# Optimization experiments

Hardware: AMD Instinct MI355X
Metric: run time of the kernel (lower is better)

Reference implementation:

```python
import jax, jax.numpy as jnp
import numpy as np

N_ELEC, N_NUC, D, F, E = 1024, 256, 64, 64, 131072
HH, HG = 128, 128
# labels: en (elec->nuc), ne (nuc->elec), same (elec->elec), anti (elec->elec)
SRC_N = [N_ELEC, N_NUC, N_ELEC, N_ELEC]
TGT_N = [N_NUC, N_ELEC, N_ELEC, N_ELEC]


def setup_inputs() -> dict:
    key = jax.random.key(0)
    ks = jax.random.split(key, 16)
    s_elec = jax.random.normal(ks[0], (N_ELEC, D), jnp.float32)
    v_elec = jax.random.normal(ks[1], (N_ELEC, D, 3), jnp.float32)
    s_nuc = jax.random.normal(ks[2], (N_NUC, D), jnp.float32)
    v_nuc = jax.random.normal(ks[3], (N_NUC, D, 3), jnp.float32)
    senders = jnp.stack([jax.random.randint(jax.random.fold_in(ks[4], i), (E,), 0, SRC_N[i]) for i in range(4)]).astype(jnp.int32)
    receivers = jnp.stack([jax.random.randint(jax.random.fold_in(ks[5], i), (E,), 0, TGT_N[i]) for i in range(4)]).astype(jnp.int32)
    dist = jax.random.uniform(ks[6], (4, E, F), jnp.float32)
    dirs = jax.random.normal(ks[7], (4, E, 3), jnp.float32)
    dirs = dirs / jnp.linalg.norm(dirs, axis=-1, keepdims=True)  # unit directions
    def w_init(k, shape):
        return jax.random.normal(k, shape, jnp.float32) / jnp.sqrt(jnp.float32(shape[-2]))
    return {
        's_elec': s_elec, 'v_elec': v_elec, 's_nuc': s_nuc, 'v_nuc': v_nuc,
        'dist': dist, 'dirs': dirs,
        'W_w': w_init(ks[8], (4, F, 3 * D)),
        'W_h1': w_init(ks[9], (4, D, HH)), 'W_h2': w_init(ks[10], (4, HH, 3 * D)),
        'W_g1': w_init(ks[11], (4, 2 * D, HG)), 'W_g2': w_init(ks[12], (4, HG, 3 * D)),
        'W_V': jnp.broadcast_to(jnp.eye(D, dtype=jnp.float32), (4, D, D)),
        'W_U': jnp.broadcast_to(jnp.eye(D, dtype=jnp.float32), (4, D, D)),
        'senders': senders, 'receivers': receivers,
    }


def _painn_layer(s_elec, v_elec, s_nuc, v_nuc, dist, dirs, W_w, W_h1, W_h2, W_g1, W_g2, W_V, W_U, senders, receivers):
    src_s = [s_elec, s_nuc, s_elec, s_elec]
    src_v = [v_elec, v_nuc, v_elec, v_elec]
    ds_e = jnp.zeros_like(s_elec); dv_e = jnp.zeros_like(v_elec)
    ds_n = jnp.zeros_like(s_nuc); dv_n = jnp.zeros_like(v_nuc)
    for i in range(4):
        n_tgt = TGT_N[i]
        # edge MLPs: w (1-layer, last linear) and h (2-layer silu, last linear), bias-free
        we = dist[i] @ W_w[i]                                   # [E, 3D]
        h_all = jax.nn.silu(src_s[i] @ W_h1[i]) @ W_h2[i]        # [n_src, 3D]
        hx = h_all[senders[i]]                                   # gather per edge
        phi_s, phi_vv, phi_vs = jnp.split(we * hx, 3, axis=-1)   # each [E, D]
        z_s = jax.ops.segment_sum(phi_s, receivers[i], n_tgt)    # [n_tgt, D]
        vv = phi_vv[..., None] * src_v[i][senders[i]]            # [E, D, 3]
        vs = phi_vs[..., None] * dirs[i][:, None, :]             # [E, D, 3]
        z_v = jax.ops.segment_sum(vv + vs, receivers[i], n_tgt)  # [n_tgt, D, 3]
        Vv = jnp.einsum('ndi,df->nfi', z_v, W_V[i])
        Uv = jnp.einsum('ndi,df->nfi', z_v, W_U[i])
        g_in = jnp.concatenate([z_s, (Vv ** 2).sum(axis=-1)], axis=-1)  # [n_tgt, 2D]
        gs = jax.nn.silu(g_in @ W_g1[i]) @ W_g2[i]               # [n_tgt, 3D]
        a_ss, a_vv, a_sv = jnp.split(gs, 3, axis=-1)
        upd_v = Uv * a_vv[..., None]
        upd_s = a_sv * jnp.einsum('nfi,nfi->nf', Uv, Vv) + a_ss
        if i == 0:  # 'en' -> nuclei
            ds_n = ds_n + upd_s; dv_n = dv_n + upd_v
        else:       # 'ne','same','anti' -> electrons
            ds_e = ds_e + upd_s; dv_e = dv_e + upd_v
    s_e = s_elec + ds_e
    v_e = v_elec + dv_e
    return jnp.concatenate([s_e, v_e.reshape(N_ELEC, -1)], axis=-1)


def reference(s_elec, v_elec, s_nuc, v_nuc, dist, dirs, W_w, W_h1, W_h2, W_g1, W_g2, W_V, W_U, senders, receivers):
    return _painn_layer(s_elec, v_elec, s_nuc, v_nuc, dist, dirs, W_w, W_h1, W_h2, W_g1, W_g2, W_V, W_U, senders, receivers)
```

## Files before the change

kernel.cpp:

```cpp
#include <hip/hip_runtime.h>
#include <stdint.h>

#define E_EDGES 131072
#define NELEC 1024
#define NNUC 256
#define MAXCHUNK 256
#define NBLK 16

typedef unsigned short ushort_t;
typedef __attribute__((ext_vector_type(8))) short short8;
typedef __attribute__((ext_vector_type(4))) short short4_t;
typedef __attribute__((ext_vector_type(4))) float float4_t;
typedef __attribute__((ext_vector_type(4))) int int4_t;
typedef __attribute__((ext_vector_type(2))) unsigned int uint2_t;

__device__ inline float silu_f(float x){ return x / (1.0f + expf(-x)); }

__device__ inline short f2bf_rne(float x){
    union { float f; uint32_t u; } a; a.f = x;
    return (short)((a.u + 0x7fffu + ((a.u >> 16) & 1u)) >> 16);
}
__device__ inline float bf2f(short h){
    union { uint32_t u; float f; } a; a.u = ((uint32_t)(uint16_t)h) << 16;
    return a.f;
}
__device__ inline ushort_t bfu(float x){ return (ushort_t)f2bf_rne(x); }
__device__ inline float asf_lo(uint32_t u){ union { uint32_t u; float f; } a; a.u = u << 16; return a.f; }
__device__ inline float asf_hi(uint32_t u){ union { uint32_t u; float f; } a; a.u = u & 0xFFFF0000u; return a.f; }

__global__ __launch_bounds__(256) void prep_kernel(
    const float* __restrict__ s_elec, const float* __restrict__ v_elec,
    const float* __restrict__ s_nuc,  const float* __restrict__ v_nuc,
    const float* __restrict__ W_h1, const float* __restrict__ W_h2,
    const float* __restrict__ W_w,
    const int* __restrict__ receivers,
    ushort_t* __restrict__ tabA, ushort_t* __restrict__ tabB,
    short* __restrict__ fragH, short* __restrict__ fragL,
    int* __restrict__ bh, float* __restrict__ out)
{
    int b = blockIdx.x, tid = threadIdx.x;
    __shared__ float sls[8][64];
    __shared__ float hidls[128][8];
    __shared__ int hist[1024];

    if (b < 288){
        int t, node0;
        if (b < 32){ t = 0; node0 = b*8; }
        else if (b < 160){ t = 1; node0 = (b-32)*8; }
        else { t = 2; node0 = (b-160)*8; }
        int tp = t + 1;
        const float* src = (t == 0) ? s_nuc : s_elec;
        const float* vsrc = (t == 0) ? v_nuc : v_elec;
        long baseA = (t == 0) ? 0 : (t == 1 ? 32768 : 163840);
        long baseB = (t == 0) ? 0 : (t == 1 ? 65536 : 327680);
        for (int i = tid; i < 512; i += 256){ int n = i >> 6, f = i & 63; sls[n][f] = src[(node0+n)*64 + f]; }
        __syncthreads();
        {
            int j = tid & 127, nh = tid >> 7;
            const float* w1 = W_h1 + (long)tp*64*128;
            float a0=0,a1=0,a2=0,a3=0;
            #pragma unroll 8
            for (int f = 0; f < 64; f++){
                float w = w1[f*128 + j];
                a0 += sls[nh*4+0][f]*w; a1 += sls[nh*4+1][f]*w;
                a2 += sls[nh*4+2][f]*w; a3 += sls[nh*4+3][f]*w;
            }
            float4_t hv = { silu_f(a0), silu_f(a1), silu_f(a2), silu_f(a3) };
            *(float4_t*)&hidls[j][nh*4] = hv;
        }
        __syncthreads();
        if (tid < 192){
            const float* w2 = W_h2 + (long)tp*128*192;
            float acc[8] = {0,0,0,0,0,0,0,0};
            #pragma unroll 4
            for (int h = 0; h < 128; h++){
                float w = w2[h*192 + tid];
                float4_t ha = *(float4_t*)&hidls[h][0];
                float4_t hb = *(float4_t*)&hidls[h][4];
                acc[0]+=ha[0]*w; acc[1]+=ha[1]*w; acc[2]+=ha[2]*w; acc[3]+=ha[3]*w;
                acc[4]+=hb[0]*w; acc[5]+=hb[1]*w; acc[6]+=hb[2]*w; acc[7]+=hb[3]*w;
            }
            int p = tid >> 6, d2 = tid & 63;
            if (p == 0){
                #pragma unroll
                for (int n = 0; n < 8; n++)
                    tabA[baseA + (long)((node0+n)*64 + d2)*2 + 0] = bfu(acc[n]);
            } else if (p == 2){
                #pragma unroll
                for (int n = 0; n < 8; n++)
                    tabA[baseA + (long)((node0+n)*64 + d2)*2 + 1] = bfu(acc[n]);
            } else {
                #pragma unroll
                for (int n = 0; n < 8; n++){
                    const float* vp = vsrc + (long)(node0+n)*192 + d2*3;
                    long o = baseB + (long)((node0+n)*64 + d2)*4;
                    tabB[o+0] = bfu(acc[n]*vp[0]);
                    tabB[o+1] = bfu(acc[n]*vp[1]);
                    tabB[o+2] = bfu(acc[n]*vp[2]);
                }
            }
        }
    } else if (b < 291){
        int t = b - 288, tp = t + 1;
        const float* W = W_w + (long)tp*64*192;
        for (int idx = tid; idx < 12288; idx += 256){
            int j    = idx & 7;
            int lane = (idx >> 3) & 63;
            int ks   = (idx >> 9) & 1;
            int nt   = idx >> 10;
            int k = ks*32 + ((lane >> 4) & 3)*8 + j;
            int n = nt*16 + (lane & 15);
            float v = W[k*192 + n];
            short hi = f2bf_rne(v);
            short lo = f2bf_rne(v - bf2f(hi));
            fragH[t*12288 + idx] = hi;
            fragL[t*12288 + idx] = lo;
        }
    } else if (b < 547){
        int i = (b - 291)*256 + tid;
        int n = i >> 6, c4 = i & 63;
        float4_t v;
        if (c4 < 16) v = *(const float4_t*)(s_elec + n*64 + c4*4);
        else         v = *(const float4_t*)(v_elec + n*192 + (c4-16)*4);
        *(float4_t*)(out + n*256 + c4*4) = v;
    } else {
        int hb = b - 547, t = hb >> 4, blk = hb & 15;
        for (int i = tid; i < 1024; i += 256) hist[i] = 0;
        __syncthreads();
        long base = (long)(t+1)*E_EDGES + blk*8192;
        #pragma unroll 4
        for (int it = 0; it < 32; it++){
            int r = receivers[base + it*256 + tid];
            atomicAdd(&hist[r], 1);
        }
        __syncthreads();
        for (int bin = tid; bin < 1024; bin += 256)
            bh[(t*1024 + bin)*NBLK + blk] = hist[bin];
    }
}

__global__ __launch_bounds__(1024) void scan_kernel(int* __restrict__ bh,
                                                    int* __restrict__ offs,
                                                    int* __restrict__ counts){
    __shared__ int buf[1024];
    int tid = threadIdx.x;
    int base = tid*48;
    int vals[48];
    const int4_t* p = (const int4_t*)(bh + base);
    int s = 0;
    #pragma unroll
    for (int j = 0; j < 12; j++){
        int4_t x = p[j];
        vals[j*4+0]=x[0]; vals[j*4+1]=x[1]; vals[j*4+2]=x[2]; vals[j*4+3]=x[3];
        s += x[0]+x[1]+x[2]+x[3];
    }
    buf[tid] = s;
    __syncthreads();
    int x = s;
    for (int off = 1; off < 1024; off <<= 1){
        int y = (tid >= off) ? buf[tid - off] : 0;
        __syncthreads();
        x += y; buf[tid] = x;
        __syncthreads();
    }
    int run = x - s;
    #pragma unroll
    for (int k = 0; k < 3; k++){
        int tb = tid*3 + k;
        offs[tb] = run;
        int c = 0;
        #pragma unroll
        for (int j = 0; j < 16; j++){
            int v = vals[k*16 + j];
            bh[base + k*16 + j] = run;
            run += v; c += v;
        }
        counts[tb] = c;
    }
}

__global__ __launch_bounds__(256) void scatter_kernel(const int* __restrict__ receivers,
                                                      const int* __restrict__ senders,
                                                      const int* __restrict__ bh,
                                                      int* __restrict__ sorted){
    int hb = blockIdx.x, t = hb >> 4, blk = hb & 15;
    int tid = threadIdx.x;
    __shared__ int cur[1024];
    for (int bin = tid; bin < 1024; bin += 256) cur[bin] = bh[(t*1024 + bin)*NBLK + blk];
    __syncthreads();
    long base = (long)(t+1)*E_EDGES + blk*8192;
    #pragma unroll 2
    for (int it = 0; it < 32; it++){
        int e = blk*8192 + it*256 + tid;
        int r = receivers[base + it*256 + tid];
        int snd = senders[base + it*256 + tid];
        int pos = atomicAdd(&cur[r], 1);
        sorted[pos] = e | (snd << 17);
    }
}

__global__ __launch_bounds__(256) void main_kernel(
    const float* __restrict__ dist, const float* __restrict__ dirs,
    const float* __restrict__ W_V, const float* __restrict__ W_U,
    const float* __restrict__ W_g1, const float* __restrict__ W_g2,
    const ushort_t* __restrict__ tabA, const ushort_t* __restrict__ tabB,
    const short* __restrict__ fragH, const short* __restrict__ fragL,
    const int* __restrict__ counts, const int* __restrict__ offs, const int* __restrict__ sorted,
    float* __restrict__ out)
{
    int b = blockIdx.x;
    int t = b >> 10, node = b & 1023, tp = t + 1;
    const ushort_t* ta = tabA + ((t == 0) ? 0 : (t == 1 ? 32768 : 163840));
    const ushort_t* tb = tabB + ((t == 0) ? 0 : (t == 1 ? 65536 : 327680));
    const float* dbase = dist + (long)tp*E_EDGES*64;
    const float* dirbase = dirs + (long)tp*E_EDGES*3;

    int tid = threadIdx.x;
    int w = tid >> 6, l = tid & 63;
    int q = l >> 4, c16 = l & 15;
    int d = w*16 + c16;

    __shared__ short AH[2][2][64][8];
    __shared__ short AL[2][2][64][8];
    __shared__ float dls[2][16][3];
    __shared__ int eid[MAXCHUNK];
    __shared__ int sid[MAXCHUNK];
    __shared__ float zs[64];
    __shared__ float zv[64][3];
    __shared__ float VvL[192], UvL[192];
    __shared__ float gin[128], hidl[128], aL[192], vdotL[64];

    short8 bhf[3][2], blf[3][2];
    #pragma unroll
    for (int ni = 0; ni < 3; ni++){
        int nt = w + ni*4;
        #pragma unroll
        for (int ks = 0; ks < 2; ks++){
            long base = (long)t*12288 + ((nt*2 + ks)*64 + l)*8;
            bhf[ni][ks] = *(const short8*)(fragH + base);
            blf[ni][ks] = *(const short8*)(fragL + base);
        }
    }

    float acc_s = 0.f, acc_v0 = 0.f, acc_v1 = 0.f, acc_v2 = 0.f;

    int deg   = counts[t*1024 + node];
    int start = offs[t*1024 + node];

    int m = tid >> 4, seg = tid & 15;
    int ks_w = seg >> 3, quad_w = (seg >> 1) & 3, j0_w = (seg & 1)*4;
    int lane2 = m | (quad_w << 4);
    int mm = tid / 3, ii = tid - mm*3;

    const float4_t z4 = {0.f,0.f,0.f,0.f};

    for (int cbase = 0; cbase < deg; cbase += MAXCHUNK){
        int chunk = deg - cbase; if (chunk > MAXCHUNK) chunk = MAXCHUNK;
        __syncthreads();
        {
            int v = 0;
            if (tid < chunk) v = sorted[(long)start + cbase + tid];
            eid[tid] = v & 131071;
            sid[tid] = ((unsigned)v) >> 17;
        }
        __syncthreads();

        int ngroups = (chunk + 15) >> 4;
        float4_t dv = z4;
        if (m < chunk) dv = *(const float4_t*)(dbase + (long)eid[m]*64 + seg*4);
        float dirv = 0.f;
        if (tid < 48 && mm < chunk) dirv = dirbase[(long)eid[mm]*3 + ii];
        uint32_t gA[4]; uint2_t gB[4];
        #pragma unroll
        for (int r = 0; r < 4; r++){
            int s = sid[q*4 + r];
            gA[r] = *(const uint32_t*)(ta + (long)(s*64 + d)*2);
            gB[r] = *(const uint2_t*)(tb + (long)(s*64 + d)*4);
        }

        for (int g = 0; g < ngroups; g++){
            int buf = g & 1;
            {
                short4_t h4, l4;
                #pragma unroll
                for (int jj = 0; jj < 4; jj++){
                    short hi = f2bf_rne(dv[jj]);
                    h4[jj] = hi;
                    l4[jj] = f2bf_rne(dv[jj] - bf2f(hi));
                }
                *(short4_t*)&AH[buf][ks_w][lane2][j0_w] = h4;
                *(short4_t*)&AL[buf][ks_w][lane2][j0_w] = l4;
                if (tid < 48) dls[buf][mm][ii] = dirv;
            }
            float4_t dvn = z4; float dirn = 0.f;
            uint32_t gAn[4] = {0,0,0,0}; uint2_t gBn[4] = {{0,0},{0,0},{0,0},{0,0}};
            if (g + 1 < ngroups){
                int li = (g+1)*16 + m;
                if (li < chunk) dvn = *(const float4_t*)(dbase + (long)eid[li]*64 + seg*4);
                int li2 = (g+1)*16 + mm;
                if (tid < 48 && li2 < chunk) dirn = dirbase[(long)eid[li2]*3 + ii];
                #pragma unroll
                for (int r = 0; r < 4; r++){
                    int s = sid[(g+1)*16 + q*4 + r];
                    gAn[r] = *(const uint32_t*)(ta + (long)(s*64 + d)*2);
                    gBn[r] = *(const uint2_t*)(tb + (long)(s*64 + d)*4);
                }
            }
            __syncthreads();

            short8 ah0 = *(short8*)&AH[buf][0][l][0];
            short8 ah1 = *(short8*)&AH[buf][1][l][0];
            short8 al0 = *(short8*)&AL[buf][0][l][0];
            short8 al1 = *(short8*)&AL[buf][1][l][0];
            float4_t C[3];
            #pragma unroll
            for (int ni = 0; ni < 3; ni++){
                float4_t acc = z4;
                acc = __builtin_amdgcn_mfma_f32_16x16x32_bf16(ah0, bhf[ni][0], acc, 0, 0, 0);
                acc = __builtin_amdgcn_mfma_f32_16x16x32_bf16(ah1, bhf[ni][1], acc, 0, 0, 0);
                acc = __builtin_amdgcn_mfma_f32_16x16x32_bf16(ah0, blf[ni][0], acc, 0, 0, 0);
                acc = __builtin_amdgcn_mfma_f32_16x16x32_bf16(ah1, blf[ni][1], acc, 0, 0, 0);
                acc = __builtin_amdgcn_mfma_f32_16x16x32_bf16(al0, bhf[ni][0], acc, 0, 0, 0);
                acc = __builtin_amdgcn_mfma_f32_16x16x32_bf16(al1, bhf[ni][1], acc, 0, 0, 0);
                C[ni] = acc;
            }

            #pragma unroll
            for (int r = 0; r < 4; r++){
                int mr = q*4 + r;
                float hs  = asf_lo(gA[r]);
                float hvs = asf_hi(gA[r]);
                float hv0 = asf_lo(gB[r][0]);
                float hv1 = asf_hi(gB[r][0]);
                float hv2 = asf_lo(gB[r][1]);
                acc_s += C[0][r] * hs;
                float pvs = C[2][r] * hvs;
                acc_v0 += C[1][r]*hv0 + pvs * dls[buf][mr][0];
                acc_v1 += C[1][r]*hv1 + pvs * dls[buf][mr][1];
                acc_v2 += C[1][r]*hv2 + pvs * dls[buf][mr][2];
            }
            dv = dvn; dirv = dirn;
            #pragma unroll
            for (int r = 0; r < 4; r++){ gA[r] = gAn[r]; gB[r] = gBn[r]; }
        }
    }

    acc_s  += __shfl_xor(acc_s, 16);  acc_s  += __shfl_xor(acc_s, 32);
    acc_v0 += __shfl_xor(acc_v0, 16); acc_v0 += __shfl_xor(acc_v0, 32);
    acc_v1 += __shfl_xor(acc_v1, 16); acc_v1 += __shfl_xor(acc_v1, 32);
    acc_v2 += __shfl_xor(acc_v2, 16); acc_v2 += __shfl_xor(acc_v2, 32);
    __syncthreads();
    if (l < 16){
        zs[d] = acc_s;
        zv[d][0] = acc_v0; zv[d][1] = acc_v1; zv[d][2] = acc_v2;
    }
    __syncthreads();

    if (tid < 192){
        int i = tid >> 6, f = tid & 63;
        const float* wv = W_V + (long)tp*64*64;
        const float* wu = W_U + (long)tp*64*64;
        float av = 0.f, au = 0.f;
        #pragma unroll 8
        for (int dd = 0; dd < 64; dd++){
            float z = zv[dd][i];
            av += z * wv[dd*64 + f];
            au += z * wu[dd*64 + f];
        }
        VvL[f*3 + i] = av;
        UvL[f*3 + i] = au;
    }
    __syncthreads();
    if (tid < 64){
        int f = tid;
        float v0 = VvL[f*3], v1 = VvL[f*3+1], v2 = VvL[f*3+2];
        float u0 = UvL[f*3], u1 = UvL[f*3+1], u2 = UvL[f*3+2];
        gin[f] = zs[f];
        gin[64 + f] = v0*v0 + v1*v1 + v2*v2;
        vdotL[f] = u0*v0 + u1*v1 + u2*v2;
    }
    __syncthreads();
    if (tid < 128){
        const float* w1 = W_g1 + (long)tp*128*128;
        float acc = 0.f;
        #pragma unroll 8
        for (int c = 0; c < 128; c++) acc += gin[c] * w1[c*128 + tid];
        hidl[tid] = silu_f(acc);
    }
    __syncthreads();
    if (tid < 192){
        const float* w2 = W_g2 + (long)tp*128*192;
        float acc = 0.f;
        #pragma unroll 8
        for (int h = 0; h < 128; h++) acc += hidl[h] * w2[h*192 + tid];
        aL[tid] = acc;
    }
    __syncthreads();
    if (tid < 64){
        int f = tid;
        float upd = aL[128 + f] * vdotL[f] + aL[f];
        atomicAdd(&out[node*256 + f], upd);
    }
    if (tid < 192){
        int i = tid >> 6, f = tid & 63;
        float updv = UvL[f*3 + i] * aL[64 + f];
        atomicAdd(&out[node*256 + 64 + f*3 + i], updv);
    }
}

extern "C" void kernel_launch(void* const* d_in, const int* in_sizes, int n_in,
                              void* d_out, int out_size, void* d_ws, size_t ws_size,
                              hipStream_t stream){
    const float* s_elec  = (const float*)d_in[0];
    const float* v_elec  = (const float*)d_in[1];
    const float* s_nuc   = (const float*)d_in[2];
    const float* v_nuc   = (const float*)d_in[3];
    const float* dist    = (const float*)d_in[4];
    const float* dirs    = (const float*)d_in[5];
    const float* W_w     = (const float*)d_in[6];
    const float* W_h1    = (const float*)d_in[7];
    const float* W_h2    = (const float*)d_in[8];
    const float* W_g1    = (const float*)d_in[9];
    const float* W_g2    = (const float*)d_in[10];
    const float* W_V     = (const float*)d_in[11];
    const float* W_U     = (const float*)d_in[12];
    const int* senders   = (const int*)d_in[13];
    const int* receivers = (const int*)d_in[14];
    float* out = (float*)d_out;
    char* ws = (char*)d_ws;

    ushort_t* tabA  = (ushort_t*)(ws + 0);
    ushort_t* tabB  = (ushort_t*)(ws + 589824);
    short* fragH  = (short*)(ws + 1769472);
    short* fragL  = (short*)(ws + 1843200);
    int*   bh     = (int*)  (ws + 1916928);
    int*   offs   = (int*)  (ws + 2113536);
    int*   counts = (int*)  (ws + 2125824);
    int*   sorted = (int*)  (ws + 2138112);
    if (ws_size < 3710976) return;

    prep_kernel<<<dim3(595), dim3(256), 0, stream>>>(
        s_elec, v_elec, s_nuc, v_nuc, W_h1, W_h2, W_w, receivers,
        tabA, tabB, fragH, fragL, bh, out);
    scan_kernel<<<dim3(1), dim3(1024), 0, stream>>>(bh, offs, counts);
    scatter_kernel<<<dim3(48), dim3(256), 0, stream>>>(receivers, senders, bh, sorted);
    main_kernel<<<dim3(3072), dim3(256), 0, stream>>>(
        dist, dirs, W_V, W_U, W_g1, W_g2,
        tabA, tabB, fragH, fragL, counts, offs, sorted, out);
}
```

Baseline: 365.3 us.

## Split main kernel into edge aggregation and batched node update kernels

Splits the per-node main kernel into two: an edge kernel that gathers and aggregates messages into a z buffer in workspace, and an update kernel that runs the V/U projections and gate MLP for four nodes per block, so each weight load is reused across nodes. The scan is also spread over three blocks, one per edge type, in place of a single block. The aim is to take the serial per-node MLP tail off the edge-heavy blocks and to amortise weight reads. In exchange it adds a kernel launch and a round trip through global memory, and the split path runs only when the workspace is large enough.

```diff
diff --git a/kernel.cpp b/kernel.cpp
--- a/kernel.cpp
+++ b/kernel.cpp
@@ -6,6 +6,7 @@
 #define NNUC 256
 #define MAXCHUNK 256
 #define NBLK 16
+#define UNPB 4
 
 typedef unsigned short ushort_t;
 typedef __attribute__((ext_vector_type(8))) short short8;
@@ -143,13 +144,14 @@
                                                     int* __restrict__ offs,
                                                     int* __restrict__ counts){
     __shared__ int buf[1024];
+    int t = blockIdx.x;
     int tid = threadIdx.x;
-    int base = tid*48;
-    int vals[48];
+    int base = (t*1024 + tid)*NBLK;
+    int vals[NBLK];
     const int4_t* p = (const int4_t*)(bh + base);
     int s = 0;
     #pragma unroll
-    for (int j = 0; j < 12; j++){
+    for (int j = 0; j < NBLK/4; j++){
         int4_t x = p[j];
         vals[j*4+0]=x[0]; vals[j*4+1]=x[1]; vals[j*4+2]=x[2]; vals[j*4+3]=x[3];
         s += x[0]+x[1]+x[2]+x[3];
@@ -163,19 +165,13 @@
         x += y; buf[tid] = x;
         __syncthreads();
     }
-    int run = x - s;
+    int run = t*E_EDGES + (x - s);
+    offs[t*1024 + tid] = run;
+    counts[t*1024 + tid] = s;
     #pragma unroll
-    for (int k = 0; k < 3; k++){
-        int tb = tid*3 + k;
-        offs[tb] = run;
-        int c = 0;
-        #pragma unroll
-        for (int j = 0; j < 16; j++){
-            int v = vals[k*16 + j];
-            bh[base + k*16 + j] = run;
-            run += v; c += v;
-        }
-        counts[tb] = c;
+    for (int j = 0; j < NBLK; j++){
+        bh[base + j] = run;
+        run += vals[j];
     }
 }
 
@@ -196,6 +192,253 @@
         int snd = senders[base + it*256 + tid];
         int pos = atomicAdd(&cur[r], 1);
         sorted[pos] = e | (snd << 17);
+    }
+}
+
+__global__ __launch_bounds__(256) void edge_kernel(
+    const float* __restrict__ dist, const float* __restrict__ dirs,
+    const ushort_t* __restrict__ tabA, const ushort_t* __restrict__ tabB,
+    const short* __restrict__ fragH, const short* __restrict__ fragL,
+    const int* __restrict__ counts, const int* __restrict__ offs, const int* __restrict__ sorted,
+    float* __restrict__ zbuf)
+{
+    int b = blockIdx.x;
+    int t = b >> 10, node = b & 1023, tp = t + 1;
+    const ushort_t* ta = tabA + ((t == 0) ? 0 : (t == 1 ? 32768 : 163840));
+    const ushort_t* tb = tabB + ((t == 0) ? 0 : (t == 1 ? 65536 : 327680));
+    const float* dbase = dist + (long)tp*E_EDGES*64;
+    const float* dirbase = dirs + (long)tp*E_EDGES*3;
+
+    int tid = threadIdx.x;
+    int w = tid >> 6, l = tid & 63;
+    int q = l >> 4, c16 = l & 15;
+    int d = w*16 + c16;
+
+    __shared__ short AH[2][2][64][8];
+    __shared__ short AL[2][2][64][8];
+    __shared__ float dls[2][16][3];
+    __shared__ int eid[MAXCHUNK];
+    __shared__ int sid[MAXCHUNK];
+
+    short8 bhf[3][2], blf[3][2];
+    #pragma unroll
+    for (int ni = 0; ni < 3; ni++){
+        int nt = w + ni*4;
+        #pragma unroll
+        for (int ks = 0; ks < 2; ks++){
+            long base = (long)t*12288 + ((nt*2 + ks)*64 + l)*8;
+            bhf[ni][ks] = *(const short8*)(fragH + base);
+            blf[ni][ks] = *(const short8*)(fragL + base);
+        }
+    }
+
+    float acc_s = 0.f, acc_v0 = 0.f, acc_v1 = 0.f, acc_v2 = 0.f;
+
+    int deg   = counts[t*1024 + node];
+    int start = offs[t*1024 + node];
+
+    int m = tid >> 4, seg = tid & 15;
+    int ks_w = seg >> 3, quad_w = (seg >> 1) & 3, j0_w = (seg & 1)*4;
+    int lane2 = m | (quad_w << 4);
+    int mm = tid / 3, ii = tid - mm*3;
+
+    const float4_t z4 = {0.f,0.f,0.f,0.f};
+
+    for (int cbase = 0; cbase < deg; cbase += MAXCHUNK){
+        int chunk = deg - cbase; if (chunk > MAXCHUNK) chunk = MAXCHUNK;
+        __syncthreads();
+        {
+            int v = 0;
+            if (tid < chunk) v = sorted[(long)start + cbase + tid];
+            eid[tid] = v & 131071;
+            sid[tid] = ((unsigned)v) >> 17;
+        }
+        __syncthreads();
+
+        int ngroups = (chunk + 15) >> 4;
+        float4_t dv = z4;
+        if (m < chunk) dv = *(const float4_t*)(dbase + (long)eid[m]*64 + seg*4);
+        float dirv = 0.f;
+        if (tid < 48 && mm < chunk) dirv = dirbase[(long)eid[mm]*3 + ii];
+        uint32_t gA[4]; uint2_t gB[4];
+        #pragma unroll
+        for (int r = 0; r < 4; r++){
+            int s = sid[q*4 + r];
+            gA[r] = *(const uint32_t*)(ta + (long)(s*64 + d)*2);
+            gB[r] = *(const uint2_t*)(tb + (long)(s*64 + d)*4);
+        }
+
+        for (int g = 0; g < ngroups; g++){
+            int buf = g & 1;
+            {
+                short4_t h4, l4;
+                #pragma unroll
+                for (int jj = 0; jj < 4; jj++){
+                    short hi = f2bf_rne(dv[jj]);
+                    h4[jj] = hi;
+                    l4[jj] = f2bf_rne(dv[jj] - bf2f(hi));
+                }
+                *(short4_t*)&AH[buf][ks_w][lane2][j0_w] = h4;
+                *(short4_t*)&AL[buf][ks_w][lane2][j0_w] = l4;
+                if (tid < 48) dls[buf][mm][ii] = dirv;
+            }
+            float4_t dvn = z4; float dirn = 0.f;
+            uint32_t gAn[4] = {0,0,0,0}; uint2_t gBn[4] = {{0,0},{0,0},{0,0},{0,0}};
+            if (g + 1 < ngroups){
+                int li = (g+1)*16 + m;
+                if (li < chunk) dvn = *(const float4_t*)(dbase + (long)eid[li]*64 + seg*4);
+                int li2 = (g+1)*16 + mm;
+                if (tid < 48 && li2 < chunk) dirn = dirbase[(long)eid[li2]*3 + ii];
+                #pragma unroll
+                for (int r = 0; r < 4; r++){
+                    int s = sid[(g+1)*16 + q*4 + r];
+                    gAn[r] = *(const uint32_t*)(ta + (long)(s*64 + d)*2);
+                    gBn[r] = *(const uint2_t*)(tb + (long)(s*64 + d)*4);
+                }
+            }
+            __syncthreads();
+
+            short8 ah0 = *(short8*)&AH[buf][0][l][0];
+            short8 ah1 = *(short8*)&AH[buf][1][l][0];
+            short8 al0 = *(short8*)&AL[buf][0][l][0];
+            short8 al1 = *(short8*)&AL[buf][1][l][0];
+            float4_t C[3];
+            #pragma unroll
+            for (int ni = 0; ni < 3; ni++){
+                float4_t acc = z4;
+                acc = __builtin_amdgcn_mfma_f32_16x16x32_bf16(ah0, bhf[ni][0], acc, 0, 0, 0);
+                acc = __builtin_amdgcn_mfma_f32_16x16x32_bf16(ah1, bhf[ni][1], acc, 0, 0, 0);
+                acc = __builtin_amdgcn_mfma_f32_16x16x32_bf16(ah0, blf[ni][0], acc, 0, 0, 0);
+                acc = __builtin_amdgcn_mfma_f32_16x16x32_bf16(ah1, blf[ni][1], acc, 0, 0, 0);
+                acc = __builtin_amdgcn_mfma_f32_16x16x32_bf16(al0, bhf[ni][0], acc, 0, 0, 0);
+                acc = __builtin_amdgcn_mfma_f32_16x16x32_bf16(al1, bhf[ni][1], acc, 0, 0, 0);
+                C[ni] = acc;
+            }
+
+            #pragma unroll
+            for (int r = 0; r < 4; r++){
+                int mr = q*4 + r;
+                float hs  = asf_lo(gA[r]);
+                float hvs = asf_hi(gA[r]);
+                float hv0 = asf_lo(gB[r][0]);
+                float hv1 = asf_hi(gB[r][0]);
+                float hv2 = asf_lo(gB[r][1]);
+                acc_s += C[0][r] * hs;
+                float pvs = C[2][r] * hvs;
+                acc_v0 += C[1][r]*hv0 + pvs * dls[buf][mr][0];
+                acc_v1 += C[1][r]*hv1 + pvs * dls[buf][mr][1];
+                acc_v2 += C[1][r]*hv2 + pvs * dls[buf][mr][2];
+            }
+            dv = dvn; dirv = dirn;
+            #pragma unroll
+            for (int r = 0; r < 4; r++){ gA[r] = gAn[r]; gB[r] = gBn[r]; }
+        }
+    }
+
+    acc_s  += __shfl_xor(acc_s, 16);  acc_s  += __shfl_xor(acc_s, 32);
+    acc_v0 += __shfl_xor(acc_v0, 16); acc_v0 += __shfl_xor(acc_v0, 32);
+    acc_v1 += __shfl_xor(acc_v1, 16); acc_v1 += __shfl_xor(acc_v1, 32);
+    acc_v2 += __shfl_xor(acc_v2, 16); acc_v2 += __shfl_xor(acc_v2, 32);
+    if (l < 16){
+        float* zp = zbuf + ((long)(t*1024 + node))*256;
+        zp[d] = acc_s;
+        zp[64 + d*3 + 0] = acc_v0;
+        zp[64 + d*3 + 1] = acc_v1;
+        zp[64 + d*3 + 2] = acc_v2;
+    }
+}
+
+__global__ __launch_bounds__(256) void update_kernel(
+    const float* __restrict__ W_V, const float* __restrict__ W_U,
+    const float* __restrict__ W_g1, const float* __restrict__ W_g2,
+    const float* __restrict__ zbuf, float* __restrict__ out)
+{
+    int b = blockIdx.x;
+    int t = b >> 8, tp = t + 1;
+    int nb = (b & 255) * UNPB;
+    int tid = threadIdx.x;
+
+    __shared__ float zls[UNPB][256];
+    __shared__ float Vv[UNPB][64][3], Uv[UNPB][64][3];
+    __shared__ float gin[UNPB][128];
+    __shared__ float hid[UNPB][128];
+    __shared__ float aL[UNPB][192];
+    __shared__ float vdot[UNPB][64];
+
+    {
+        int n = tid >> 6, c = tid & 63;
+        *(float4_t*)&zls[n][c*4] =
+            *(const float4_t*)(zbuf + ((long)(t*1024 + nb + n))*256 + c*4);
+    }
+    __syncthreads();
+
+    {
+        int f = tid & 63, n = tid >> 6;
+        const float* wv = W_V + (long)tp*4096;
+        const float* wu = W_U + (long)tp*4096;
+        float av0=0,av1=0,av2=0,au0=0,au1=0,au2=0;
+        #pragma unroll 4
+        for (int dd = 0; dd < 64; dd++){
+            float wvv = wv[dd*64 + f], wuu = wu[dd*64 + f];
+            float z0 = zls[n][64 + dd*3 + 0];
+            float z1 = zls[n][64 + dd*3 + 1];
+            float z2 = zls[n][64 + dd*3 + 2];
+            av0 += z0*wvv; av1 += z1*wvv; av2 += z2*wvv;
+            au0 += z0*wuu; au1 += z1*wuu; au2 += z2*wuu;
+        }
+        Vv[n][f][0]=av0; Vv[n][f][1]=av1; Vv[n][f][2]=av2;
+        Uv[n][f][0]=au0; Uv[n][f][1]=au1; Uv[n][f][2]=au2;
+    }
+    __syncthreads();
+
+    {
+        int n = tid >> 6, f = tid & 63;
+        float v0=Vv[n][f][0], v1=Vv[n][f][1], v2=Vv[n][f][2];
+        float u0=Uv[n][f][0], u1=Uv[n][f][1], u2=Uv[n][f][2];
+        gin[n][f]      = zls[n][f];
+        gin[n][64 + f] = v0*v0 + v1*v1 + v2*v2;
+        vdot[n][f]     = u0*v0 + u1*v1 + u2*v2;
+    }
+    __syncthreads();
+
+    {
+        int h = tid & 127, ng = tid >> 7;
+        const float* w1 = W_g1 + (long)tp*16384;
+        float a0=0, a1=0;
+        #pragma unroll 4
+        for (int c = 0; c < 128; c++){
+            float w = w1[c*128 + h];
+            a0 += gin[ng*2+0][c]*w;
+            a1 += gin[ng*2+1][c]*w;
+        }
+        hid[ng*2+0][h] = silu_f(a0);
+        hid[ng*2+1][h] = silu_f(a1);
+    }
+    __syncthreads();
+
+    if (tid < 192){
+        const float* w2 = W_g2 + (long)tp*24576;
+        float a0=0,a1=0,a2=0,a3=0;
+        #pragma unroll 4
+        for (int h = 0; h < 128; h++){
+            float w = w2[h*192 + tid];
+            a0 += hid[0][h]*w; a1 += hid[1][h]*w;
+            a2 += hid[2][h]*w; a3 += hid[3][h]*w;
+        }
+        aL[0][tid]=a0; aL[1][tid]=a1; aL[2][tid]=a2; aL[3][tid]=a3;
+    }
+    __syncthreads();
+
+    {
+        int n = tid >> 6, f = tid & 63;
+        float upd = aL[n][128 + f]*vdot[n][f] + aL[n][f];
+        atomicAdd(&out[(nb + n)*256 + f], upd);
+        float g = aL[n][64 + f];
+        #pragma unroll
+        for (int i = 0; i < 3; i++){
+            float updv = Uv[n][f][i] * g;
+            atomicAdd(&out[(nb + n)*256 + 64 + f*3 + i], updv);
+        }
     }
 }
 
@@ -228,7 +471,7 @@
     __shared__ float zs[64];
     __shared__ float zv[64][3];
     __shared__ float VvL[192], UvL[192];
-    __shared__ float gin[128], hidl[128], aL[192], vdotL[64];
+    __shared__ float gin[128], hidl[128], aLrr[192], vdotL[64];
 
     short8 bhf[3][2], blf[3][2];
     #pragma unroll
@@ -393,17 +636,17 @@
         float acc = 0.f;
         #pragma unroll 8
         for (int h = 0; h < 128; h++) acc += hidl[h] * w2[h*192 + tid];
-        aL[tid] = acc;
+        aLrr[tid] = acc;
     }
     __syncthreads();
     if (tid < 64){
         int f = tid;
-        float upd = aL[128 + f] * vdotL[f] + aL[f];
+        float upd = aLrr[128 + f] * vdotL[f] + aLrr[f];
         atomicAdd(&out[node*256 + f], upd);
     }
     if (tid < 192){
         int i = tid >> 6, f = tid & 63;
-        float updv = UvL[f*3 + i] * aL[64 + f];
+        float updv = UvL[f*3 + i] * aLrr[64 + f];
         atomicAdd(&out[node*256 + 64 + f*3 + i], updv);
     }
 }
@@ -437,14 +680,23 @@
     int*   offs   = (int*)  (ws + 2113536);
     int*   counts = (int*)  (ws + 2125824);
     int*   sorted = (int*)  (ws + 2138112);
+    float* zbuf   = (float*)(ws + 3710976);
     if (ws_size < 3710976) return;
+    bool split = (ws_size >= 6856704);
 
     prep_kernel<<<dim3(595), dim3(256), 0, stream>>>(
         s_elec, v_elec, s_nuc, v_nuc, W_h1, W_h2, W_w, receivers,
         tabA, tabB, fragH, fragL, bh, out);
-    scan_kernel<<<dim3(1), dim3(1024), 0, stream>>>(bh, offs, counts);
+    scan_kernel<<<dim3(3), dim3(1024), 0, stream>>>(bh, offs, counts);
     scatter_kernel<<<dim3(48), dim3(256), 0, stream>>>(receivers, senders, bh, sorted);
-    main_kernel<<<dim3(3072), dim3(256), 0, stream>>>(
-        dist, dirs, W_V, W_U, W_g1, W_g2,
-        tabA, tabB, fragH, fragL, counts, offs, sorted, out);
-}
+    if (split){
+        edge_kernel<<<dim3(3072), dim3(256), 0, stream>>>(
+            dist, dirs, tabA, tabB, fragH, fragL, counts, offs, sorted, zbuf);
+        update_kernel<<<dim3(768), dim3(256), 0, stream>>>(
+            W_V, W_U, W_g1, W_g2, zbuf, out);
+    } else {
+        main_kernel<<<dim3(3072), dim3(256), 0, stream>>>(
+            dist, dirs, W_V, W_U, W_g1, W_g2,
+            tabA, tabB, fragH, fragL, counts, offs, sorted, out);
+    }
+}
```

New measurement: 339.4 us. 1.08x faster.
